# Optimization experiments

Hardware: AMD Instinct MI355X
Metric: run time of the kernel (lower is better)

Reference implementation:

```python
import jax, jax.numpy as jnp
import numpy as np

# Config (matches BlockConfig defaults for linear attention)
B, S, D = 2, 4096, 2048
H, KVH, HD, CK = 16, 8, 128, 4   # n_heads, n_kv_heads, head_dim, conv_kernel
DQK, DV = KVH * HD, H * HD       # 1024, 2048
EPS = 1e-6


def setup_inputs() -> dict:
    key = jax.random.key(0)
    ks = jax.random.split(key, 12)
    std = 0.02
    return {
        "x": jax.random.normal(ks[0], (B, S, D), jnp.float32),
        "wq": jax.random.normal(ks[1], (DQK, D), jnp.float32) * std,
        "wk": jax.random.normal(ks[2], (DQK, D), jnp.float32) * std,
        "wv": jax.random.normal(ks[3], (DV, D), jnp.float32) * std,
        "wo": jax.random.normal(ks[4], (D, DV), jnp.float32) * std,
        "q_conv_w": jax.random.normal(ks[5], (DQK, 1, CK), jnp.float32) * std,
        "k_conv_w": jax.random.normal(ks[6], (DQK, 1, CK), jnp.float32) * std,
        "alpha_w": jax.random.normal(ks[7], (H, D), jnp.float32) * std,
        "alpha_b": jnp.zeros((H,), jnp.float32),
        "beta_w": jax.random.normal(ks[8], (H, D), jnp.float32) * std,
        "beta_b": jnp.zeros((H,), jnp.float32),
        "g_w": jax.random.normal(ks[9], (DV, D), jnp.float32) * std,
        "norm_q_w": jnp.ones((HD,), jnp.float32),
        "norm_k_w": jnp.ones((HD,), jnp.float32),
    }


def _rmsnorm(x, w):
    # normalize over last dim (head_dim) in fp32, elementwise affine, no bias
    xf = x.astype(jnp.float32)
    var = jnp.mean(xf * xf, axis=-1, keepdims=True)
    return (w * xf * jax.lax.rsqrt(var + EPS)).astype(x.dtype)


def _causal_dwconv(x, w):
    # x: (B, S, C); w: (C, 1, k) depthwise; torch Conv1d padding=k-1 then [:S]
    # == left-pad (k-1, 0) cross-correlation
    y = jax.lax.conv_general_dilated(
        x.transpose(0, 2, 1), w, window_strides=(1,),
        padding=[(CK - 1, 0)], feature_group_count=w.shape[0],
        dimension_numbers=("NCH", "OIH", "NCH"))
    return y.transpose(0, 2, 1)


def reference(x, wq, wk, wv, wo, q_conv_w, k_conv_w,
              alpha_w, alpha_b, beta_w, beta_b, g_w, norm_q_w, norm_k_w):
    Q = x @ wq.T                              # (B,S,DQK)
    K = x @ wk.T                              # (B,S,DQK)
    V = x @ wv.T                              # (B,S,DV)
    Q = _causal_dwconv(Q, q_conv_w)
    K = _causal_dwconv(K, k_conv_w)
    Q = _rmsnorm(Q.reshape(B, S, KVH, HD), norm_q_w)
    K = _rmsnorm(K.reshape(B, S, KVH, HD), norm_k_w)
    V = V.reshape(B, S, H, HD)
    alpha = jax.nn.sigmoid(x @ alpha_w.T + alpha_b)              # (B,S,H)
    beta = jax.nn.sigmoid(x @ beta_w.T + beta_b) / (HD ** 0.5)   # (B,S,H)
    rep = H // KVH
    Q = jnp.repeat(Q, rep, axis=2)            # (B,S,H,HD)
    K = jnp.repeat(K, rep, axis=2)

    # time-major for scan
    Qt = Q.transpose(1, 0, 2, 3)
    Kt = K.transpose(1, 0, 2, 3)
    Vt = V.transpose(1, 0, 2, 3)
    at = alpha.transpose(1, 0, 2)
    bt = beta.transpose(1, 0, 2)

    S0 = jnp.zeros((B, H, HD, HD), x.dtype)

    def step(S_state, inp):
        q_t, k_t, v_t, a_t, b_t = inp
        pred = jnp.einsum("bhd,bhdv->bhv", k_t, S_state)
        delta = v_t - pred
        update = jnp.einsum("bhv,bhd->bhdv", delta, k_t)
        S_state = a_t[:, :, None, None] * S_state + b_t[:, :, None, None] * update
        o_t = jnp.einsum("bhd,bhdv->bhv", q_t, S_state)
        return S_state, o_t

    _, O = jax.lax.scan(step, S0, (Qt, Kt, Vt, at, bt))  # O: (S,B,H,HD)
    out = O.transpose(1, 0, 2, 3).reshape(B, S, DV)
    g = jax.nn.sigmoid(x @ g_w.T)
    return (g * out) @ wo.T
```

## Files before the change

kernel.cpp:

```cpp
#include <hip/hip_runtime.h>
#include <stdint.h>

#define DEV static __device__ __forceinline__

typedef __bf16 bf16x8 __attribute__((ext_vector_type(8)));
typedef float f32x4 __attribute__((ext_vector_type(4)));

constexpr int Bc = 2, Sc = 4096, Dc = 2048, Hc = 16, KVHc = 8, HDc = 128;
constexpr int DQKc = 1024, DVc = 2048;
constexpr int Mc = Bc * Sc;
constexpr int NCATc = 6144;
constexpr int CT = 64;
constexpr int NCH = Sc / CT;
constexpr int COEF_STRIDE = 16896;
constexpr float EPSc = 1e-6f;

DEV uint16_t f2bf(float f) {
  uint32_t u = __float_as_uint(f);
  u += 0x7FFFu + ((u >> 16) & 1u);
  return (uint16_t)(u >> 16);
}
DEV float bf2f(uint16_t h) { return __uint_as_float(((uint32_t)h) << 16); }
DEV float sigmoidf_(float z) { return 1.0f / (1.0f + __expf(-z)); }

DEV void gload16(void* lds, const void* g) {
  auto gp = (const __attribute__((address_space(1))) uint32_t*)(uintptr_t)g;
  auto lp = (__attribute__((address_space(3))) uint32_t*)(uint32_t)(uintptr_t)lds;
  __builtin_amdgcn_global_load_lds(gp, lp, 16, 0, 0);
}

__global__ __launch_bounds__(256) void cast_kernel(const float* __restrict__ src,
                                                   uint16_t* __restrict__ dst, int n4) {
  int i = blockIdx.x * blockDim.x + threadIdx.x;
  int stride = gridDim.x * blockDim.x;
  for (; i < n4; i += stride) {
    float4 v = *(const float4*)(src + (size_t)i * 4);
    ushort4 o;
    o.x = f2bf(v.x); o.y = f2bf(v.y); o.z = f2bf(v.z); o.w = f2bf(v.w);
    *(ushort4*)(dst + (size_t)i * 4) = o;
  }
}

template <typename OutT>
__global__ __launch_bounds__(512, 2) void gemm256_bt(const uint16_t* __restrict__ A,
                                                     const uint16_t* __restrict__ Bw,
                                                     OutT* __restrict__ C, int Ndim, int Kdim) {
  __shared__ uint16_t sT[2][2][2][8192];

  const int nbn = Ndim / 256;
  const int nwg = gridDim.x;
  int q = nwg >> 3, r = nwg & 7;
  int xcd = blockIdx.x & 7, lin = blockIdx.x >> 3;
  int swz = (xcd < r ? xcd * (q + 1) : r * (q + 1) + (xcd - r) * q) + lin;
  const int bm = swz / nbn, bn = swz % nbn;

  const int tid = threadIdx.x;
  const int wid = tid >> 6, lane = tid & 63;
  const int wm = wid >> 2, wn = wid & 3;
  const int lr = lane & 15;
  const int sswz8 = (((lane >> 4) ^ (lr & 3)) * 8);
  const int arow_base = wm * 128 + lr;
  const int brow_base = wn * 64 + lr;

  const uint16_t* Ab = A + (size_t)(bm * 256) * Kdim;
  const uint16_t* Bb = Bw + (size_t)(bn * 256) * Kdim;
  const int NT = Kdim >> 6;

  int srowA[2], srowB_dummy;
  (void)srowB_dummy;
  int soff[2];
  const int wbase = tid & ~63;
#pragma unroll
  for (int u = 0; u < 2; ++u) {
    int L = u * 512 + tid;
    srowA[u] = L >> 2;
    soff[u] = (((L & 3) ^ ((L >> 2) & 3)) * 8);
  }

  auto STAGE = [&](int buf, int mat, int kh, int kt) {
    const uint16_t* gb = mat == 0 ? Ab : Bb;
    uint16_t* rg = &sT[buf][mat][kh][0];
#pragma unroll
    for (int u = 0; u < 2; ++u) {
      const uint16_t* g = gb + (size_t)srowA[u] * Kdim + kt * 64 + kh * 32 + soff[u];
      gload16(rg + (u * 512 + wbase) * 8, g);
    }
  };

  f32x4 acc[8][4] = {};
  bf16x8 bfr[4];

  STAGE(0, 0, 0, 0); STAGE(0, 1, 0, 0);
  STAGE(0, 0, 1, 0); STAGE(0, 1, 1, 0);
  STAGE(1, 0, 0, 1); STAGE(1, 1, 0, 1);
  asm volatile("s_waitcnt vmcnt(4)" ::: "memory");
  __builtin_amdgcn_s_barrier();

  for (int kt = 0; kt < NT; ++kt) {
    const int buf = kt & 1;
    const uint16_t* aR0 = &sT[buf][0][0][0];
    const uint16_t* bR0 = &sT[buf][1][0][0];
    const uint16_t* aR1 = &sT[buf][0][1][0];
    const uint16_t* bR1 = &sT[buf][1][1][0];

    {
      bf16x8 af[4];
#pragma unroll
      for (int m = 0; m < 4; ++m)
        af[m] = *(const bf16x8*)&aR0[(arow_base + m * 16) * 32 + sswz8];
#pragma unroll
      for (int n = 0; n < 4; ++n)
        bfr[n] = *(const bf16x8*)&bR0[(brow_base + n * 16) * 32 + sswz8];
      if (kt + 1 < NT) STAGE(buf ^ 1, 0, 1, kt + 1);
      __builtin_amdgcn_s_setprio(1);
#pragma unroll
      for (int m = 0; m < 4; ++m)
#pragma unroll
        for (int n = 0; n < 4; ++n)
          acc[m][n] = __builtin_amdgcn_mfma_f32_16x16x32_bf16(af[m], bfr[n], acc[m][n], 0, 0, 0);
      __builtin_amdgcn_s_setprio(0);
      __builtin_amdgcn_s_barrier();
    }
    {
      bf16x8 af[4];
#pragma unroll
      for (int m = 0; m < 4; ++m)
        af[m] = *(const bf16x8*)&aR0[(arow_base + (m + 4) * 16) * 32 + sswz8];
      if (kt + 1 < NT) STAGE(buf ^ 1, 1, 1, kt + 1);
      __builtin_amdgcn_s_setprio(1);
#pragma unroll
      for (int m = 0; m < 4; ++m)
#pragma unroll
        for (int n = 0; n < 4; ++n)
          acc[m + 4][n] = __builtin_amdgcn_mfma_f32_16x16x32_bf16(af[m], bfr[n], acc[m + 4][n], 0, 0, 0);
      __builtin_amdgcn_s_setprio(0);
      __builtin_amdgcn_s_barrier();
    }
    {
      bf16x8 af[4];
#pragma unroll
      for (int m = 0; m < 4; ++m)
        af[m] = *(const bf16x8*)&aR1[(arow_base + m * 16) * 32 + sswz8];
#pragma unroll
      for (int n = 0; n < 4; ++n)
        bfr[n] = *(const bf16x8*)&bR1[(brow_base + n * 16) * 32 + sswz8];
      if (kt + 2 < NT) STAGE(buf, 0, 0, kt + 2);
      __builtin_amdgcn_s_setprio(1);
#pragma unroll
      for (int m = 0; m < 4; ++m)
#pragma unroll
        for (int n = 0; n < 4; ++n)
          acc[m][n] = __builtin_amdgcn_mfma_f32_16x16x32_bf16(af[m], bfr[n], acc[m][n], 0, 0, 0);
      __builtin_amdgcn_s_setprio(0);
      __builtin_amdgcn_s_barrier();
    }
    {
      bf16x8 af[4];
#pragma unroll
      for (int m = 0; m < 4; ++m)
        af[m] = *(const bf16x8*)&aR1[(arow_base + (m + 4) * 16) * 32 + sswz8];
      if (kt + 2 < NT) STAGE(buf, 1, 0, kt + 2);
      __builtin_amdgcn_s_setprio(1);
#pragma unroll
      for (int m = 0; m < 4; ++m)
#pragma unroll
        for (int n = 0; n < 4; ++n)
          acc[m + 4][n] = __builtin_amdgcn_mfma_f32_16x16x32_bf16(af[m], bfr[n], acc[m + 4][n], 0, 0, 0);
      __builtin_amdgcn_s_setprio(0);
    }
    if (kt + 1 < NT) {
      if (kt + 2 < NT)
        asm volatile("s_waitcnt vmcnt(4)" ::: "memory");
      else
        asm volatile("s_waitcnt vmcnt(0)" ::: "memory");
      __builtin_amdgcn_s_barrier();
    }
  }

  const int r0 = (lane >> 4) * 4;
#pragma unroll
  for (int m = 0; m < 8; ++m)
#pragma unroll
    for (int n = 0; n < 4; ++n) {
      int col = bn * 256 + wn * 64 + n * 16 + lr;
#pragma unroll
      for (int j = 0; j < 4; ++j) {
        int row = bm * 256 + wm * 128 + m * 16 + r0 + j;
        float val = acc[m][n][j];
        if constexpr (sizeof(OutT) == 2)
          C[(size_t)row * Ndim + col] = (OutT)f2bf(val);
        else
          C[(size_t)row * Ndim + col] = (OutT)val;
      }
    }
}

__global__ __launch_bounds__(256) void alphabeta_kernel(const float* __restrict__ x,
                                                        const float* __restrict__ aw,
                                                        const float* __restrict__ abias,
                                                        const float* __restrict__ bw,
                                                        const float* __restrict__ bbias,
                                                        float* __restrict__ out) {
  __shared__ float xrow[Dc];
  const int row = blockIdx.x;
  const float* xp = x + (size_t)row * Dc;
  for (int i = threadIdx.x; i < Dc; i += 256) xrow[i] = xp[i];
  __syncthreads();
  const int o = threadIdx.x >> 3, lg = threadIdx.x & 7;
  const float* wrow = (o < 16) ? (aw + (size_t)o * Dc) : (bw + (size_t)(o - 16) * Dc);
  float s = 0.f;
  for (int i = lg * 4; i < Dc; i += 32) {
    float4 xv = *(const float4*)&xrow[i];
    float4 wv = *(const float4*)&wrow[i];
    s += xv.x * wv.x + xv.y * wv.y + xv.z * wv.z + xv.w * wv.w;
  }
  s += __shfl_xor(s, 1); s += __shfl_xor(s, 2); s += __shfl_xor(s, 4);
  if (lg == 0) {
    float bias = (o < 16) ? abias[o] : bbias[o - 16];
    float sig = sigmoidf_(s + bias);
    if (o >= 16) sig *= 0.08838834764831845f;
    out[(size_t)row * 32 + o] = sig;
  }
}

__global__ __launch_bounds__(256) void convnorm_kernel(const uint16_t* __restrict__ C1,
                                                       const float* __restrict__ qcw,
                                                       const float* __restrict__ kcw,
                                                       const float* __restrict__ nqw,
                                                       const float* __restrict__ nkw,
                                                       uint16_t* __restrict__ Qn,
                                                       uint16_t* __restrict__ Kn) {
  const int wid = blockIdx.x * 4 + (threadIdx.x >> 6);
  const int lane = threadIdx.x & 63;
  const int kvh = wid & 7;
  const int t = (wid >> 3) & (Sc - 1);
  const int b = wid >> 15;
  float qv[2], kv[2];
#pragma unroll
  for (int half = 0; half < 2; ++half) {
    const int c = lane + half * 64;
    const int ch = kvh * HDc + c;
    float qs = 0.f, ks = 0.f;
#pragma unroll
    for (int j = 0; j < 4; ++j) {
      int tt = t - 3 + j;
      if (tt >= 0) {
        size_t rb = (size_t)(b * Sc + tt) * NCATc;
        qs = fmaf(bf2f(C1[rb + ch]), qcw[ch * 4 + j], qs);
        ks = fmaf(bf2f(C1[rb + 1024 + ch]), kcw[ch * 4 + j], ks);
      }
    }
    qv[half] = qs; kv[half] = ks;
  }
  float sq = qv[0] * qv[0] + qv[1] * qv[1];
  float sk = kv[0] * kv[0] + kv[1] * kv[1];
#pragma unroll
  for (int m = 1; m < 64; m <<= 1) { sq += __shfl_xor(sq, m); sk += __shfl_xor(sk, m); }
  const float rq = rsqrtf(sq * (1.f / HDc) + EPSc);
  const float rk = rsqrtf(sk * (1.f / HDc) + EPSc);
#pragma unroll
  for (int half = 0; half < 2; ++half) {
    const int c = lane + half * 64;
    size_t oidx = (size_t)(b * Sc + t) * DQKc + kvh * HDc + c;
    Qn[oidx] = f2bf(nqw[c] * qv[half] * rq);
    Kn[oidx] = f2bf(nkw[c] * kv[half] * rk);
  }
}

__global__ __launch_bounds__(256) void scores_kernel(const uint16_t* __restrict__ Qn,
                                                     const uint16_t* __restrict__ Kn,
                                                     const float* __restrict__ ab,
                                                     uint8_t* __restrict__ coef) {
  __shared__ __align__(16) char smem[72192];
  uint16_t* sK = (uint16_t*)smem;
  float* Wtf = (float*)smem;
  uint16_t* sQ = (uint16_t*)(smem + 17408);
  uint16_t* sM2 = sQ;
  uint16_t* Msh = (uint16_t*)(smem + 34816);
  uint16_t* Msl = (uint16_t*)(smem + 44032);
  uint16_t* Thh = (uint16_t*)(smem + 53248);
  uint16_t* Thl = (uint16_t*)(smem + 62464);
  float* Lb = (float*)(smem + 71680);
  float* bbv = Lb + 64;

  const int bid = blockIdx.x;
  const int c = bid & 63, h = (bid >> 6) & 15, b = bid >> 10;
  const int kh = h >> 1;
  const int t0 = c * 64;
  const int tid = threadIdx.x;
  const int w = tid >> 6, l = tid & 63, lr = l & 15, lk = (l >> 4) * 8;
  const int sr = tid >> 2, sq2 = tid & 3;

  uint8_t* cbase = coef + (size_t)((b * Hc + h) * NCH + c) * COEF_STRIDE;
  uint16_t* m2out = (uint16_t*)cbase;
  uint16_t* eout = (uint16_t*)(cbase + 8192);
  float* gout = (float*)(cbase + 16384);

  {
    const size_t rb = (size_t)(b * Sc + t0 + sr) * DQKc + kh * HDc + sq2 * 32;
#pragma unroll
    for (int u = 0; u < 4; ++u) {
      uint4 kv = *(const uint4*)(Kn + rb + u * 8);
      uint4 qv = *(const uint4*)(Qn + rb + u * 8);
      *(uint4*)&sK[sr * 136 + sq2 * 32 + u * 8] = kv;
      *(uint4*)&sQ[sr * 136 + sq2 * 32 + u * 8] = qv;
    }
  }
  if (tid < 64) {
    const float* abp = ab + (size_t)(b * Sc + t0 + tid) * 32 + h;
    float av = fmaxf(abp[0], 1e-30f);
    float bv = abp[16];
    float la = log2f(av);
    float L = la;
#pragma unroll
    for (int off = 1; off < 64; off <<= 1) {
      float up = __shfl_up(L, off, 64);
      if (tid >= off) L += up;
    }
    Lb[tid] = L; bbv[tid] = bv;
    gout[tid] = exp2f(L - la);
    gout[64 + tid] = exp2f(L);
  }
  __syncthreads();

  f32x4 kkacc[4] = {}, qkacc[4] = {};
#pragma unroll
  for (int k0 = 0; k0 < 128; k0 += 32) {
    bf16x8 ka = *(const bf16x8*)&sK[(16 * w + lr) * 136 + k0 + lk];
    bf16x8 qa = *(const bf16x8*)&sQ[(16 * w + lr) * 136 + k0 + lk];
#pragma unroll
    for (int n = 0; n < 4; ++n) {
      bf16x8 kb = *(const bf16x8*)&sK[(16 * n + lr) * 136 + k0 + lk];
      kkacc[n] = __builtin_amdgcn_mfma_f32_16x16x32_bf16(ka, kb, kkacc[n], 0, 0, 0);
      qkacc[n] = __builtin_amdgcn_mfma_f32_16x16x32_bf16(qa, kb, qkacc[n], 0, 0, 0);
    }
  }
  __syncthreads();

  const float L63 = Lb[63];
#pragma unroll
  for (int n = 0; n < 4; ++n)
#pragma unroll
    for (int jj = 0; jj < 4; ++jj) {
      const int i = 16 * w + (l >> 4) * 4 + jj;
      const int j = 16 * n + lr;
      float Li = Lb[i];
      float Lim = (i > 0) ? Lb[(i > 0) ? i - 1 : 0] : 0.f;
      float Lj = Lb[j];
      float bj = bbv[j];
      float wv = (j < i) ? exp2f(Lim - Lj) * bj * kkacc[n][jj] : 0.f;
      Wtf[j * 68 + i] = wv;
      float ms = (j <= i) ? exp2f(Li - Lj) * bj * qkacc[n][jj] : 0.f;
      uint16_t mh = f2bf(ms);
      Msh[i * 72 + j] = mh;
      Msl[i * 72 + j] = f2bf(ms - bf2f(mh));
    }
  __syncthreads();

  if (tid < 64) {
    float acc[64];
#pragma unroll
    for (int i = 0; i < 64; ++i) acc[i] = 0.f;
#pragma unroll
    for (int ll = 0; ll < 64; ++ll) {
      float xl = ((tid == ll) ? 1.f : 0.f) - acc[ll];
      uint16_t xh = f2bf(xl);
      Thh[tid * 72 + ll] = xh;
      Thl[tid * 72 + ll] = f2bf(xl - bf2f(xh));
#pragma unroll
      for (int i = ll + 1; i < 64; ++i)
        acc[i] = fmaf(Wtf[ll * 68 + i], xl, acc[i]);
    }
  }
  __syncthreads();

  f32x4 m2acc[4] = {};
#pragma unroll
  for (int k0 = 0; k0 < 64; k0 += 32) {
    bf16x8 ah = *(const bf16x8*)&Msh[(16 * w + lr) * 72 + k0 + lk];
    bf16x8 al = *(const bf16x8*)&Msl[(16 * w + lr) * 72 + k0 + lk];
#pragma unroll
    for (int n = 0; n < 4; ++n) {
      bf16x8 bh = *(const bf16x8*)&Thh[(16 * n + lr) * 72 + k0 + lk];
      bf16x8 bl = *(const bf16x8*)&Thl[(16 * n + lr) * 72 + k0 + lk];
      m2acc[n] = __builtin_amdgcn_mfma_f32_16x16x32_bf16(ah, bh, m2acc[n], 0, 0, 0);
      m2acc[n] = __builtin_amdgcn_mfma_f32_16x16x32_bf16(ah, bl, m2acc[n], 0, 0, 0);
      m2acc[n] = __builtin_amdgcn_mfma_f32_16x16x32_bf16(al, bh, m2acc[n], 0, 0, 0);
    }
  }
#pragma unroll
  for (int n = 0; n < 4; ++n)
#pragma unroll
    for (int jj = 0; jj < 4; ++jj) {
      const int i = 16 * w + (l >> 4) * 4 + jj;
      const int j = 16 * n + lr;
      sM2[i * 72 + j] = f2bf(m2acc[n][jj]);
    }
  {
    const int i2 = tid >> 2, tq = tid & 3;
    float gC = exp2f(L63 - Lb[i2]) * bbv[i2];
    uint32_t pk[8];
#pragma unroll
    for (int p = 0; p < 8; ++p) {
      int t1 = tq * 16 + p * 2;
      float e0 = gC * (bf2f(Thh[(t1 + 0) * 72 + i2]) + bf2f(Thl[(t1 + 0) * 72 + i2]));
      float e1 = gC * (bf2f(Thh[(t1 + 1) * 72 + i2]) + bf2f(Thl[(t1 + 1) * 72 + i2]));
      pk[p] = (uint32_t)f2bf(e0) | ((uint32_t)f2bf(e1) << 16);
    }
    uint4 o0 = make_uint4(pk[0], pk[1], pk[2], pk[3]);
    uint4 o1 = make_uint4(pk[4], pk[5], pk[6], pk[7]);
    *(uint4*)(eout + i2 * 64 + tq * 16) = o0;
    *(uint4*)(eout + i2 * 64 + tq * 16 + 8) = o1;
  }
  __syncthreads();
  {
    const int i2 = tid >> 2, tq = tid & 3;
    uint4 a0 = *(const uint4*)&sM2[i2 * 72 + tq * 16];
    uint4 a1 = *(const uint4*)&sM2[i2 * 72 + tq * 16 + 8];
    *(uint4*)(m2out + i2 * 64 + tq * 16) = a0;
    *(uint4*)(m2out + i2 * 64 + tq * 16 + 8) = a1;
  }
}

__global__ __launch_bounds__(256) void scan_kernel(const uint16_t* __restrict__ Qn,
                                                   const uint16_t* __restrict__ Kn,
                                                   const uint16_t* __restrict__ C1,
                                                   const uint8_t* __restrict__ coef,
                                                   float* __restrict__ O) {
  __shared__ __align__(16) uint16_t Kb[64 * 136];
  __shared__ __align__(16) uint16_t Qb[64 * 136];
  __shared__ __align__(16) uint16_t Ktb[128 * 72];
  __shared__ __align__(16) uint16_t M2b[64 * 72];
  __shared__ __align__(16) uint16_t Eb[64 * 72];
  __shared__ __align__(16) uint16_t Vb[64 * 24];
  __shared__ __align__(16) uint16_t Rt[16 * 72];
  __shared__ __align__(16) uint16_t D2t[16 * 72];
  __shared__ __align__(16) uint16_t Sh[16 * 136];
  __shared__ __align__(16) uint16_t Slo[16 * 136];
  __shared__ float gABb[128];

  const int bid = blockIdx.x;
  const int kh = bid & 7;
  const int j2 = bid >> 3;
  const int sl = j2 >> 2;
  const int b = (j2 >> 1) & 1;
  const int h = kh * 2 + (j2 & 1);
  const int ch0 = (b * Hc + h) * NCH;

  const int tid = threadIdx.x;
  const int w = tid >> 6, l = tid & 63;
  const int lr = l & 15, lk = (l >> 4) * 8;
  const int row0 = 16 * w + (l >> 4) * 4;
  const int vcol = lr;
  const int sr = tid >> 2, sq2 = tid & 3;

  const size_t kqbase = (size_t)(b * Sc) * DQKc + kh * HDc;
  const size_t vbase = (size_t)(b * Sc) * NCATc + 2048 + h * HDc + sl * 16;
  float* Ob = O + (size_t)(b * Sc) * DVc + h * HDc + sl * 16 + vcol;

  float sreg[2][4] = {};
  uint4 kA[4], kB[4], qA[4], qB[4];

  auto LOADS = [&](int cn, uint4 (&kd)[4], uint4 (&qd)[4], uint4 (&m2d)[2], uint4 (&ed)[2],
                   uint4& vd, float& gd) {
    const size_t rb = kqbase + (size_t)(cn * CT + sr) * DQKc + sq2 * 32;
#pragma unroll
    for (int u = 0; u < 4; ++u) {
      kd[u] = *(const uint4*)(Kn + rb + u * 8);
      qd[u] = *(const uint4*)(Qn + rb + u * 8);
    }
    const uint16_t* cf = (const uint16_t*)(coef + (size_t)(ch0 + cn) * COEF_STRIDE);
#pragma unroll
    for (int e = 0; e < 2; ++e) {
      m2d[e] = *(const uint4*)(cf + sr * 64 + sq2 * 16 + e * 8);
      ed[e] = *(const uint4*)(cf + 4096 + sr * 64 + sq2 * 16 + e * 8);
    }
    if (tid < 128) {
      vd = *(const uint4*)(C1 + vbase + (size_t)(cn * CT + (tid >> 1)) * NCATc + (tid & 1) * 8);
      gd = ((const float*)(cf + 8192))[tid];
    }
  };
  auto WSTAGE = [&](const uint4 (&kd)[4], const uint4 (&qd)[4], const uint4 (&m2d)[2],
                    const uint4 (&ed)[2], const uint4& vd, const float& gd) {
#pragma unroll
    for (int u = 0; u < 4; ++u) {
      *(uint4*)&Kb[sr * 136 + sq2 * 32 + u * 8] = kd[u];
      *(uint4*)&Qb[sr * 136 + sq2 * 32 + u * 8] = qd[u];
    }
#pragma unroll
    for (int e = 0; e < 2; ++e) {
      *(uint4*)&M2b[sr * 72 + sq2 * 16 + e * 8] = m2d[e];
      *(uint4*)&Eb[sr * 72 + sq2 * 16 + e * 8] = ed[e];
    }
    if (tid < 128) {
      *(uint4*)&Vb[(tid >> 1) * 24 + (tid & 1) * 8] = vd;
      gABb[tid] = gd;
    }
  };

  auto CHUNK = [&](int c, bool pre, uint4 (&kcur)[4], uint4 (&knxt)[4],
                   uint4 (&qcur)[4], uint4 (&qnxt)[4]) {
    uint4 m2d[2], ed[2]; uint4 vd; float gd = 0.f;
    if (pre) LOADS(c + 1, knxt, qnxt, m2d, ed, vd, gd);

#pragma unroll
    for (int u = 0; u < 4; ++u) {
      const int c0 = sq2 * 32 + u * 8;
      uint32_t x0 = kcur[u].x, x1 = kcur[u].y, x2 = kcur[u].z, x3 = kcur[u].w;
      Ktb[(c0 + 0) * 72 + sr] = (uint16_t)x0; Ktb[(c0 + 1) * 72 + sr] = (uint16_t)(x0 >> 16);
      Ktb[(c0 + 2) * 72 + sr] = (uint16_t)x1; Ktb[(c0 + 3) * 72 + sr] = (uint16_t)(x1 >> 16);
      Ktb[(c0 + 4) * 72 + sr] = (uint16_t)x2; Ktb[(c0 + 5) * 72 + sr] = (uint16_t)(x2 >> 16);
      Ktb[(c0 + 6) * 72 + sr] = (uint16_t)x3; Ktb[(c0 + 7) * 72 + sr] = (uint16_t)(x3 >> 16);
    }
    f32x4 accP = {0, 0, 0, 0}, accPq = {0, 0, 0, 0};
#pragma unroll
    for (int k0 = 0; k0 < 128; k0 += 32) {
      bf16x8 ka = *(const bf16x8*)&Kb[(16 * w + lr) * 136 + k0 + lk];
      bf16x8 qa = *(const bf16x8*)&Qb[(16 * w + lr) * 136 + k0 + lk];
      bf16x8 shf = *(const bf16x8*)&Sh[lr * 136 + k0 + lk];
      bf16x8 slf = *(const bf16x8*)&Slo[lr * 136 + k0 + lk];
      accP = __builtin_amdgcn_mfma_f32_16x16x32_bf16(ka, shf, accP, 0, 0, 0);
      accP = __builtin_amdgcn_mfma_f32_16x16x32_bf16(ka, slf, accP, 0, 0, 0);
      accPq = __builtin_amdgcn_mfma_f32_16x16x32_bf16(qa, shf, accPq, 0, 0, 0);
      accPq = __builtin_amdgcn_mfma_f32_16x16x32_bf16(qa, slf, accPq, 0, 0, 0);
    }
    {
      float rv[4];
#pragma unroll
      for (int j = 0; j < 4; ++j) {
        float vv = bf2f(Vb[(row0 + j) * 24 + vcol]);
        float ga = gABb[row0 + j];
        rv[j] = vv - ga * accP[j];
      }
      uint32_t r01 = (uint32_t)f2bf(rv[0]) | ((uint32_t)f2bf(rv[1]) << 16);
      uint32_t r23 = (uint32_t)f2bf(rv[2]) | ((uint32_t)f2bf(rv[3]) << 16);
      *(uint2*)&Rt[vcol * 72 + row0] = make_uint2(r01, r23);
    }
    __syncthreads();

    f32x4 accD2 = {0, 0, 0, 0}, accO = {0, 0, 0, 0};
#pragma unroll
    for (int k0 = 0; k0 < 64; k0 += 32) {
      bf16x8 rb8 = *(const bf16x8*)&Rt[lr * 72 + k0 + lk];
      bf16x8 ea = *(const bf16x8*)&Eb[(16 * w + lr) * 72 + k0 + lk];
      bf16x8 ma = *(const bf16x8*)&M2b[(16 * w + lr) * 72 + k0 + lk];
      accD2 = __builtin_amdgcn_mfma_f32_16x16x32_bf16(ea, rb8, accD2, 0, 0, 0);
      accO = __builtin_amdgcn_mfma_f32_16x16x32_bf16(ma, rb8, accO, 0, 0, 0);
    }
    {
      float* op = Ob + (size_t)(c * CT) * DVc;
#pragma unroll
      for (int j = 0; j < 4; ++j) {
        float o = gABb[64 + row0 + j] * accPq[j] + accO[j];
        op[(size_t)(row0 + j) * DVc] = o;
      }
      uint32_t d01 = (uint32_t)f2bf(accD2[0]) | ((uint32_t)f2bf(accD2[1]) << 16);
      uint32_t d23 = (uint32_t)f2bf(accD2[2]) | ((uint32_t)f2bf(accD2[3]) << 16);
      *(uint2*)&D2t[vcol * 72 + row0] = make_uint2(d01, d23);
    }
    __syncthreads();

    const float gT = gABb[127];
    f32x4 accY[2] = {{0, 0, 0, 0}, {0, 0, 0, 0}};
#pragma unroll
    for (int k0 = 0; k0 < 64; k0 += 32) {
      bf16x8 db = *(const bf16x8*)&D2t[lr * 72 + k0 + lk];
      bf16x8 ka0 = *(const bf16x8*)&Ktb[(32 * w + lr) * 72 + k0 + lk];
      bf16x8 ka1 = *(const bf16x8*)&Ktb[(32 * w + 16 + lr) * 72 + k0 + lk];
      accY[0] = __builtin_amdgcn_mfma_f32_16x16x32_bf16(ka0, db, accY[0], 0, 0, 0);
      accY[1] = __builtin_amdgcn_mfma_f32_16x16x32_bf16(ka1, db, accY[1], 0, 0, 0);
    }
#pragma unroll
    for (int m = 0; m < 2; ++m) {
      uint16_t hi[4], lo[4];
#pragma unroll
      for (int j = 0; j < 4; ++j) {
        float s = gT * sreg[m][j] + accY[m][j];
        sreg[m][j] = s;
        hi[j] = f2bf(s);
        lo[j] = f2bf(s - bf2f(hi[j]));
      }
      const int dk0 = 32 * w + m * 16 + (l >> 4) * 4;
      *(uint2*)&Sh[vcol * 136 + dk0] =
          make_uint2((uint32_t)hi[0] | ((uint32_t)hi[1] << 16),
                     (uint32_t)hi[2] | ((uint32_t)hi[3] << 16));
      *(uint2*)&Slo[vcol * 136 + dk0] =
          make_uint2((uint32_t)lo[0] | ((uint32_t)lo[1] << 16),
                     (uint32_t)lo[2] | ((uint32_t)lo[3] << 16));
    }
    if (pre) WSTAGE(knxt, qnxt, m2d, ed, vd, gd);
    __syncthreads();
  };

  {
    uint4 m2d[2], ed[2]; uint4 vd; float gd = 0.f;
    LOADS(0, kA, qA, m2d, ed, vd, gd);
    WSTAGE(kA, qA, m2d, ed, vd, gd);
  }
  for (int i = tid; i < 16 * 136; i += 256) { Sh[i] = 0; Slo[i] = 0; }
  __syncthreads();

  for (int c2 = 0; c2 < NCH; c2 += 2) {
    CHUNK(c2, true, kA, kB, qA, qB);
    CHUNK(c2 + 1, c2 + 2 < NCH, kB, kA, qB, qA);
  }
}

__global__ __launch_bounds__(256) void gmul_kernel(const uint16_t* __restrict__ C1,
                                                   const float* __restrict__ O,
                                                   uint16_t* __restrict__ gOb) {
  int i = blockIdx.x * blockDim.x + threadIdx.x;
  const int n4 = Mc * DVc / 4;
  const int stride = gridDim.x * blockDim.x;
  for (; i < n4; i += stride) {
    int idx = i * 4;
    int row = idx >> 11;
    int col = idx & (DVc - 1);
    ushort4 gr = *(const ushort4*)&C1[(size_t)row * NCATc + 4096 + col];
    float4 ov = *(const float4*)&O[idx];
    ushort4 r;
    r.x = f2bf(sigmoidf_(bf2f(gr.x)) * ov.x);
    r.y = f2bf(sigmoidf_(bf2f(gr.y)) * ov.y);
    r.z = f2bf(sigmoidf_(bf2f(gr.z)) * ov.z);
    r.w = f2bf(sigmoidf_(bf2f(gr.w)) * ov.w);
    *(ushort4*)&gOb[idx] = r;
  }
}

extern "C" void kernel_launch(void* const* d_in, const int* in_sizes, int n_in,
                              void* d_out, int out_size, void* d_ws, size_t ws_size,
                              hipStream_t stream) {
  (void)in_sizes; (void)n_in; (void)out_size; (void)ws_size;
  const float* x     = (const float*)d_in[0];
  const float* wq    = (const float*)d_in[1];
  const float* wk    = (const float*)d_in[2];
  const float* wv    = (const float*)d_in[3];
  const float* wo    = (const float*)d_in[4];
  const float* qcw   = (const float*)d_in[5];
  const float* kcw   = (const float*)d_in[6];
  const float* aw    = (const float*)d_in[7];
  const float* abias = (const float*)d_in[8];
  const float* bw    = (const float*)d_in[9];
  const float* bbias = (const float*)d_in[10];
  const float* gw    = (const float*)d_in[11];
  const float* nqw   = (const float*)d_in[12];
  const float* nkw   = (const float*)d_in[13];

  uint8_t* ws = (uint8_t*)d_ws;
  uint16_t* xb   = (uint16_t*)(ws);
  uint16_t* wcat = (uint16_t*)(ws + 33554432);
  uint16_t* wob  = (uint16_t*)(ws + 58720256);
  uint16_t* c1   = (uint16_t*)(ws + 67108864);
  float*    abuf = (float*)   (ws + 167772160);
  uint16_t* qn   = (uint16_t*)(ws + 168820736);
  uint16_t* kn   = (uint16_t*)(ws + 185597952);
  uint8_t*  cofs = (uint8_t*)ws;
  uint16_t* gob  = xb;
  float* obuf = (float*)d_out;

  cast_kernel<<<2048, 256, 0, stream>>>(x, xb, Mc * Dc / 4);
  cast_kernel<<<1024, 256, 0, stream>>>(wq, wcat, DQKc * Dc / 4);
  cast_kernel<<<1024, 256, 0, stream>>>(wk, wcat + DQKc * Dc, DQKc * Dc / 4);
  cast_kernel<<<1024, 256, 0, stream>>>(wv, wcat + 2 * DQKc * Dc, DVc * Dc / 4);
  cast_kernel<<<1024, 256, 0, stream>>>(gw, wcat + 2 * DQKc * Dc + DVc * Dc, DVc * Dc / 4);
  cast_kernel<<<1024, 256, 0, stream>>>(wo, wob, DVc * Dc / 4);

  gemm256_bt<uint16_t><<<768, 512, 0, stream>>>(xb, wcat, c1, NCATc, Dc);
  alphabeta_kernel<<<8192, 256, 0, stream>>>(x, aw, abias, bw, bbias, abuf);
  convnorm_kernel<<<16384, 256, 0, stream>>>(c1, qcw, kcw, nqw, nkw, qn, kn);
  scores_kernel<<<2048, 256, 0, stream>>>(qn, kn, abuf, cofs);
  scan_kernel<<<256, 256, 0, stream>>>(qn, kn, c1, cofs, obuf);
  gmul_kernel<<<2048, 256, 0, stream>>>(c1, obuf, gob);
  gemm256_bt<float><<<256, 512, 0, stream>>>(gob, wob, (float*)d_out, DVc, Dc);
}
```

Measured before the change: 791.6 us.

## Fuse gating into scan, share K across head pairs, double-buffer K transpose

The sigmoid gate multiply moves into the scan kernel's output path, which writes bf16 gated output in place over the g columns of C1. The final GEMM reads those columns directly through a new lda stride, so gmul_kernel and the fp32 O round trip go away. scores_kernel now handles both query heads that share one KV head per block, loading Q/K once and using more LDS. alphabeta processes 8 rows per block. The scan double-buffers the K transpose scatter and overlaps it with MFMA work, and the GEMM LDS swizzle pattern is changed. These changes add LDS pressure and strided 2-byte gate loads inside the scan.

```diff
diff --git a/kernel.cpp b/kernel.cpp
--- a/kernel.cpp
+++ b/kernel.cpp
@@ -44,7 +44,8 @@
 template <typename OutT>
 __global__ __launch_bounds__(512, 2) void gemm256_bt(const uint16_t* __restrict__ A,
                                                      const uint16_t* __restrict__ Bw,
-                                                     OutT* __restrict__ C, int Ndim, int Kdim) {
+                                                     OutT* __restrict__ C, int Ndim, int Kdim,
+                                                     int lda) {
   __shared__ uint16_t sT[2][2][2][8192];
 
   const int nbn = Ndim / 256;
@@ -58,31 +59,31 @@
   const int wid = tid >> 6, lane = tid & 63;
   const int wm = wid >> 2, wn = wid & 3;
   const int lr = lane & 15;
-  const int sswz8 = (((lane >> 4) ^ (lr & 3)) * 8);
+  const int sswz8 = (((lane >> 4) ^ ((lr >> 1) & 3)) * 8);
   const int arow_base = wm * 128 + lr;
   const int brow_base = wn * 64 + lr;
 
-  const uint16_t* Ab = A + (size_t)(bm * 256) * Kdim;
+  const uint16_t* Ab = A + (size_t)(bm * 256) * lda;
   const uint16_t* Bb = Bw + (size_t)(bn * 256) * Kdim;
   const int NT = Kdim >> 6;
 
-  int srowA[2], srowB_dummy;
-  (void)srowB_dummy;
+  int srowA[2];
   int soff[2];
   const int wbase = tid & ~63;
 #pragma unroll
   for (int u = 0; u < 2; ++u) {
     int L = u * 512 + tid;
     srowA[u] = L >> 2;
-    soff[u] = (((L & 3) ^ ((L >> 2) & 3)) * 8);
+    soff[u] = (((L & 3) ^ ((L >> 3) & 3)) * 8);
   }
 
   auto STAGE = [&](int buf, int mat, int kh, int kt) {
     const uint16_t* gb = mat == 0 ? Ab : Bb;
+    const int ld = mat == 0 ? lda : Kdim;
     uint16_t* rg = &sT[buf][mat][kh][0];
 #pragma unroll
     for (int u = 0; u < 2; ++u) {
-      const uint16_t* g = gb + (size_t)srowA[u] * Kdim + kt * 64 + kh * 32 + soff[u];
+      const uint16_t* g = gb + (size_t)srowA[u] * ld + kt * 64 + kh * 32 + soff[u];
       gload16(rg + (u * 512 + wbase) * 8, g);
     }
   };
@@ -201,26 +202,26 @@
                                                         const float* __restrict__ bw,
                                                         const float* __restrict__ bbias,
                                                         float* __restrict__ out) {
-  __shared__ float xrow[Dc];
-  const int row = blockIdx.x;
-  const float* xp = x + (size_t)row * Dc;
-  for (int i = threadIdx.x; i < Dc; i += 256) xrow[i] = xp[i];
+  __shared__ float xs[8 * Dc];
+  const int row0 = blockIdx.x * 8;
+  const float* xp = x + (size_t)row0 * Dc;
+  for (int i = threadIdx.x; i < 8 * Dc / 4; i += 256)
+    *(float4*)&xs[i * 4] = *(const float4*)(xp + (size_t)i * 4);
   __syncthreads();
-  const int o = threadIdx.x >> 3, lg = threadIdx.x & 7;
+  const int r = threadIdx.x >> 5, o = threadIdx.x & 31;
   const float* wrow = (o < 16) ? (aw + (size_t)o * Dc) : (bw + (size_t)(o - 16) * Dc);
+  const float* xr = &xs[r * Dc];
   float s = 0.f;
-  for (int i = lg * 4; i < Dc; i += 32) {
-    float4 xv = *(const float4*)&xrow[i];
-    float4 wv = *(const float4*)&wrow[i];
+#pragma unroll 4
+  for (int k = 0; k < Dc; k += 4) {
+    float4 wv = *(const float4*)(wrow + k);
+    float4 xv = *(const float4*)(xr + k);
     s += xv.x * wv.x + xv.y * wv.y + xv.z * wv.z + xv.w * wv.w;
   }
-  s += __shfl_xor(s, 1); s += __shfl_xor(s, 2); s += __shfl_xor(s, 4);
-  if (lg == 0) {
-    float bias = (o < 16) ? abias[o] : bbias[o - 16];
-    float sig = sigmoidf_(s + bias);
-    if (o >= 16) sig *= 0.08838834764831845f;
-    out[(size_t)row * 32 + o] = sig;
-  }
+  float bias = (o < 16) ? abias[o] : bbias[o - 16];
+  float sig = sigmoidf_(s + bias);
+  if (o >= 16) sig *= 0.08838834764831845f;
+  out[(size_t)(row0 + r) * 32 + o] = sig;
 }
 
 __global__ __launch_bounds__(256) void convnorm_kernel(const uint16_t* __restrict__ C1,
@@ -271,30 +272,29 @@
                                                      const uint16_t* __restrict__ Kn,
                                                      const float* __restrict__ ab,
                                                      uint8_t* __restrict__ coef) {
-  __shared__ __align__(16) char smem[72192];
+  __shared__ __align__(16) char smem[109568];
   uint16_t* sK = (uint16_t*)smem;
-  float* Wtf = (float*)smem;
   uint16_t* sQ = (uint16_t*)(smem + 17408);
-  uint16_t* sM2 = sQ;
-  uint16_t* Msh = (uint16_t*)(smem + 34816);
-  uint16_t* Msl = (uint16_t*)(smem + 44032);
-  uint16_t* Thh = (uint16_t*)(smem + 53248);
-  uint16_t* Thl = (uint16_t*)(smem + 62464);
-  float* Lb = (float*)(smem + 71680);
-  float* bbv = Lb + 64;
+  uint16_t* sM2 = (uint16_t*)smem;
+  float* Lb = (float*)(smem + 108544);
+  float* bbv = Lb + 128;
+
+  auto Wt_p  = [&](int hd) { return (float*)(smem + hd * 17408); };
+  auto Msh_p = [&](int hd) { return (uint16_t*)(smem + 34816 + hd * 18432); };
+  auto Msl_p = [&](int hd) { return (uint16_t*)(smem + 44032 + hd * 18432); };
+  auto Thh_p = [&](int hd) { return (uint16_t*)(smem + 71680 + hd * 18432); };
+  auto Thl_p = [&](int hd) { return (uint16_t*)(smem + 80896 + hd * 18432); };
 
   const int bid = blockIdx.x;
-  const int c = bid & 63, h = (bid >> 6) & 15, b = bid >> 10;
-  const int kh = h >> 1;
+  const int c = bid & 63, kh = (bid >> 6) & 7, b = bid >> 9;
   const int t0 = c * 64;
   const int tid = threadIdx.x;
   const int w = tid >> 6, l = tid & 63, lr = l & 15, lk = (l >> 4) * 8;
   const int sr = tid >> 2, sq2 = tid & 3;
 
-  uint8_t* cbase = coef + (size_t)((b * Hc + h) * NCH + c) * COEF_STRIDE;
-  uint16_t* m2out = (uint16_t*)cbase;
-  uint16_t* eout = (uint16_t*)(cbase + 8192);
-  float* gout = (float*)(cbase + 16384);
+  auto cb_p = [&](int hd) {
+    return coef + (size_t)((b * Hc + kh * 2 + hd) * NCH + c) * COEF_STRIDE;
+  };
 
   {
     const size_t rb = (size_t)(b * Sc + t0 + sr) * DQKc + kh * HDc + sq2 * 32;
@@ -306,8 +306,9 @@
       *(uint4*)&sQ[sr * 136 + sq2 * 32 + u * 8] = qv;
     }
   }
-  if (tid < 64) {
-    const float* abp = ab + (size_t)(b * Sc + t0 + tid) * 32 + h;
+  if (tid < 128) {
+    const int hd = tid >> 6, tt = tid & 63;
+    const float* abp = ab + (size_t)(b * Sc + t0 + tt) * 32 + (kh * 2 + hd);
     float av = fmaxf(abp[0], 1e-30f);
     float bv = abp[16];
     float la = log2f(av);
@@ -315,11 +316,12 @@
 #pragma unroll
     for (int off = 1; off < 64; off <<= 1) {
       float up = __shfl_up(L, off, 64);
-      if (tid >= off) L += up;
-    }
-    Lb[tid] = L; bbv[tid] = bv;
-    gout[tid] = exp2f(L - la);
-    gout[64 + tid] = exp2f(L);
+      if (tt >= off) L += up;
+    }
+    Lb[hd * 64 + tt] = L; bbv[hd * 64 + tt] = bv;
+    float* gout = (float*)(cb_p(hd) + 16384);
+    gout[tt] = exp2f(L - la);
+    gout[64 + tt] = exp2f(L);
   }
   __syncthreads();
 
@@ -337,99 +339,121 @@
   }
   __syncthreads();
 
-  const float L63 = Lb[63];
-#pragma unroll
-  for (int n = 0; n < 4; ++n)
-#pragma unroll
-    for (int jj = 0; jj < 4; ++jj) {
-      const int i = 16 * w + (l >> 4) * 4 + jj;
-      const int j = 16 * n + lr;
-      float Li = Lb[i];
-      float Lim = (i > 0) ? Lb[(i > 0) ? i - 1 : 0] : 0.f;
-      float Lj = Lb[j];
-      float bj = bbv[j];
-      float wv = (j < i) ? exp2f(Lim - Lj) * bj * kkacc[n][jj] : 0.f;
-      Wtf[j * 68 + i] = wv;
-      float ms = (j <= i) ? exp2f(Li - Lj) * bj * qkacc[n][jj] : 0.f;
-      uint16_t mh = f2bf(ms);
-      Msh[i * 72 + j] = mh;
-      Msl[i * 72 + j] = f2bf(ms - bf2f(mh));
-    }
+#pragma unroll
+  for (int hd = 0; hd < 2; ++hd) {
+    float* Wt = Wt_p(hd);
+    uint16_t* Mh = Msh_p(hd);
+    uint16_t* Ml = Msl_p(hd);
+    const float* Lh = Lb + hd * 64;
+    const float* bh = bbv + hd * 64;
+#pragma unroll
+    for (int n = 0; n < 4; ++n)
+#pragma unroll
+      for (int jj = 0; jj < 4; ++jj) {
+        const int i = 16 * w + (l >> 4) * 4 + jj;
+        const int j = 16 * n + lr;
+        float Li = Lh[i];
+        float Lim = (i > 0) ? Lh[(i > 0) ? i - 1 : 0] : 0.f;
+        float Lj = Lh[j];
+        float bj = bh[j];
+        float wv = (j < i) ? exp2f(Lim - Lj) * bj * kkacc[n][jj] : 0.f;
+        Wt[j * 68 + i] = wv;
+        float ms = (j <= i) ? exp2f(Li - Lj) * bj * qkacc[n][jj] : 0.f;
+        uint16_t mh = f2bf(ms);
+        Mh[i * 72 + j] = mh;
+        Ml[i * 72 + j] = f2bf(ms - bf2f(mh));
+      }
+  }
   __syncthreads();
 
-  if (tid < 64) {
+  if (tid < 128) {
+    const int hd = tid >> 6, col = tid & 63;
+    float* Wt = Wt_p(hd);
+    uint16_t* Th = Thh_p(hd);
+    uint16_t* Tl = Thl_p(hd);
     float acc[64];
 #pragma unroll
     for (int i = 0; i < 64; ++i) acc[i] = 0.f;
 #pragma unroll
     for (int ll = 0; ll < 64; ++ll) {
-      float xl = ((tid == ll) ? 1.f : 0.f) - acc[ll];
+      float xl = ((col == ll) ? 1.f : 0.f) - acc[ll];
       uint16_t xh = f2bf(xl);
-      Thh[tid * 72 + ll] = xh;
-      Thl[tid * 72 + ll] = f2bf(xl - bf2f(xh));
+      Th[col * 72 + ll] = xh;
+      Tl[col * 72 + ll] = f2bf(xl - bf2f(xh));
 #pragma unroll
       for (int i = ll + 1; i < 64; ++i)
-        acc[i] = fmaf(Wtf[ll * 68 + i], xl, acc[i]);
+        acc[i] = fmaf(Wt[ll * 68 + i], xl, acc[i]);
     }
   }
   __syncthreads();
 
-  f32x4 m2acc[4] = {};
-#pragma unroll
-  for (int k0 = 0; k0 < 64; k0 += 32) {
-    bf16x8 ah = *(const bf16x8*)&Msh[(16 * w + lr) * 72 + k0 + lk];
-    bf16x8 al = *(const bf16x8*)&Msl[(16 * w + lr) * 72 + k0 + lk];
-#pragma unroll
-    for (int n = 0; n < 4; ++n) {
-      bf16x8 bh = *(const bf16x8*)&Thh[(16 * n + lr) * 72 + k0 + lk];
-      bf16x8 bl = *(const bf16x8*)&Thl[(16 * n + lr) * 72 + k0 + lk];
-      m2acc[n] = __builtin_amdgcn_mfma_f32_16x16x32_bf16(ah, bh, m2acc[n], 0, 0, 0);
-      m2acc[n] = __builtin_amdgcn_mfma_f32_16x16x32_bf16(ah, bl, m2acc[n], 0, 0, 0);
-      m2acc[n] = __builtin_amdgcn_mfma_f32_16x16x32_bf16(al, bh, m2acc[n], 0, 0, 0);
-    }
-  }
-#pragma unroll
-  for (int n = 0; n < 4; ++n)
-#pragma unroll
-    for (int jj = 0; jj < 4; ++jj) {
-      const int i = 16 * w + (l >> 4) * 4 + jj;
-      const int j = 16 * n + lr;
-      sM2[i * 72 + j] = f2bf(m2acc[n][jj]);
-    }
-  {
-    const int i2 = tid >> 2, tq = tid & 3;
-    float gC = exp2f(L63 - Lb[i2]) * bbv[i2];
-    uint32_t pk[8];
-#pragma unroll
-    for (int p = 0; p < 8; ++p) {
-      int t1 = tq * 16 + p * 2;
-      float e0 = gC * (bf2f(Thh[(t1 + 0) * 72 + i2]) + bf2f(Thl[(t1 + 0) * 72 + i2]));
-      float e1 = gC * (bf2f(Thh[(t1 + 1) * 72 + i2]) + bf2f(Thl[(t1 + 1) * 72 + i2]));
-      pk[p] = (uint32_t)f2bf(e0) | ((uint32_t)f2bf(e1) << 16);
-    }
-    uint4 o0 = make_uint4(pk[0], pk[1], pk[2], pk[3]);
-    uint4 o1 = make_uint4(pk[4], pk[5], pk[6], pk[7]);
-    *(uint4*)(eout + i2 * 64 + tq * 16) = o0;
-    *(uint4*)(eout + i2 * 64 + tq * 16 + 8) = o1;
-  }
-  __syncthreads();
-  {
-    const int i2 = tid >> 2, tq = tid & 3;
-    uint4 a0 = *(const uint4*)&sM2[i2 * 72 + tq * 16];
-    uint4 a1 = *(const uint4*)&sM2[i2 * 72 + tq * 16 + 8];
-    *(uint4*)(m2out + i2 * 64 + tq * 16) = a0;
-    *(uint4*)(m2out + i2 * 64 + tq * 16 + 8) = a1;
+  for (int hd = 0; hd < 2; ++hd) {
+    uint16_t* Mh = Msh_p(hd);
+    uint16_t* Ml = Msl_p(hd);
+    uint16_t* Th = Thh_p(hd);
+    uint16_t* Tl = Thl_p(hd);
+    uint16_t* m2out = (uint16_t*)cb_p(hd);
+    uint16_t* eout = (uint16_t*)(cb_p(hd) + 8192);
+    const float* Lh = Lb + hd * 64;
+    const float* bh = bbv + hd * 64;
+    const float L63 = Lh[63];
+
+    {
+      const int i2 = tid >> 2, tq = tid & 3;
+      float gC = exp2f(L63 - Lh[i2]) * bh[i2];
+      uint32_t pk[8];
+#pragma unroll
+      for (int p = 0; p < 8; ++p) {
+        int t1 = tq * 16 + p * 2;
+        float e0 = gC * (bf2f(Th[(t1 + 0) * 72 + i2]) + bf2f(Tl[(t1 + 0) * 72 + i2]));
+        float e1 = gC * (bf2f(Th[(t1 + 1) * 72 + i2]) + bf2f(Tl[(t1 + 1) * 72 + i2]));
+        pk[p] = (uint32_t)f2bf(e0) | ((uint32_t)f2bf(e1) << 16);
+      }
+      *(uint4*)(eout + i2 * 64 + tq * 16) = make_uint4(pk[0], pk[1], pk[2], pk[3]);
+      *(uint4*)(eout + i2 * 64 + tq * 16 + 8) = make_uint4(pk[4], pk[5], pk[6], pk[7]);
+    }
+
+    f32x4 m2acc[4] = {};
+#pragma unroll
+    for (int k0 = 0; k0 < 64; k0 += 32) {
+      bf16x8 ah = *(const bf16x8*)&Mh[(16 * w + lr) * 72 + k0 + lk];
+      bf16x8 al = *(const bf16x8*)&Ml[(16 * w + lr) * 72 + k0 + lk];
+#pragma unroll
+      for (int n = 0; n < 4; ++n) {
+        bf16x8 bhf = *(const bf16x8*)&Th[(16 * n + lr) * 72 + k0 + lk];
+        bf16x8 blf = *(const bf16x8*)&Tl[(16 * n + lr) * 72 + k0 + lk];
+        m2acc[n] = __builtin_amdgcn_mfma_f32_16x16x32_bf16(ah, bhf, m2acc[n], 0, 0, 0);
+        m2acc[n] = __builtin_amdgcn_mfma_f32_16x16x32_bf16(ah, blf, m2acc[n], 0, 0, 0);
+        m2acc[n] = __builtin_amdgcn_mfma_f32_16x16x32_bf16(al, bhf, m2acc[n], 0, 0, 0);
+      }
+    }
+#pragma unroll
+    for (int n = 0; n < 4; ++n)
+#pragma unroll
+      for (int jj = 0; jj < 4; ++jj) {
+        const int i = 16 * w + (l >> 4) * 4 + jj;
+        const int j = 16 * n + lr;
+        sM2[i * 72 + j] = f2bf(m2acc[n][jj]);
+      }
+    __syncthreads();
+    {
+      const int i2 = tid >> 2, tq = tid & 3;
+      uint4 a0 = *(const uint4*)&sM2[i2 * 72 + tq * 16];
+      uint4 a1 = *(const uint4*)&sM2[i2 * 72 + tq * 16 + 8];
+      *(uint4*)(m2out + i2 * 64 + tq * 16) = a0;
+      *(uint4*)(m2out + i2 * 64 + tq * 16 + 8) = a1;
+    }
+    __syncthreads();
   }
 }
 
 __global__ __launch_bounds__(256) void scan_kernel(const uint16_t* __restrict__ Qn,
                                                    const uint16_t* __restrict__ Kn,
-                                                   const uint16_t* __restrict__ C1,
-                                                   const uint8_t* __restrict__ coef,
-                                                   float* __restrict__ O) {
+                                                   uint16_t* C1,
+                                                   const uint8_t* __restrict__ coef) {
   __shared__ __align__(16) uint16_t Kb[64 * 136];
   __shared__ __align__(16) uint16_t Qb[64 * 136];
-  __shared__ __align__(16) uint16_t Ktb[128 * 72];
+  __shared__ __align__(16) uint16_t Ktb[2][128 * 72];
   __shared__ __align__(16) uint16_t M2b[64 * 72];
   __shared__ __align__(16) uint16_t Eb[64 * 72];
   __shared__ __align__(16) uint16_t Vb[64 * 24];
@@ -456,13 +480,14 @@
 
   const size_t kqbase = (size_t)(b * Sc) * DQKc + kh * HDc;
   const size_t vbase = (size_t)(b * Sc) * NCATc + 2048 + h * HDc + sl * 16;
-  float* Ob = O + (size_t)(b * Sc) * DVc + h * HDc + sl * 16 + vcol;
+  uint16_t* Gb = C1 + (size_t)(b * Sc) * NCATc + 4096 + h * HDc + sl * 16 + vcol;
 
   float sreg[2][4] = {};
   uint4 kA[4], kB[4], qA[4], qB[4];
+  ushort4 gv0, gv1;
 
   auto LOADS = [&](int cn, uint4 (&kd)[4], uint4 (&qd)[4], uint4 (&m2d)[2], uint4 (&ed)[2],
-                   uint4& vd, float& gd) {
+                   uint4& vd, float& gd, ushort4& gvd) {
     const size_t rb = kqbase + (size_t)(cn * CT + sr) * DQKc + sq2 * 32;
 #pragma unroll
     for (int u = 0; u < 4; ++u) {
@@ -479,6 +504,11 @@
       vd = *(const uint4*)(C1 + vbase + (size_t)(cn * CT + (tid >> 1)) * NCATc + (tid & 1) * 8);
       gd = ((const float*)(cf + 8192))[tid];
     }
+    const uint16_t* gpre = Gb + (size_t)(cn * CT) * NCATc;
+    gvd.x = gpre[(size_t)(row0 + 0) * NCATc];
+    gvd.y = gpre[(size_t)(row0 + 1) * NCATc];
+    gvd.z = gpre[(size_t)(row0 + 2) * NCATc];
+    gvd.w = gpre[(size_t)(row0 + 3) * NCATc];
   };
   auto WSTAGE = [&](const uint4 (&kd)[4], const uint4 (&qd)[4], const uint4 (&m2d)[2],
                     const uint4 (&ed)[2], const uint4& vd, const float& gd) {
@@ -497,21 +527,22 @@
       gABb[tid] = gd;
     }
   };
+  auto SCAT = [&](uint16_t* Kt, const uint4 (&kd)[4], int u) {
+    const int c0 = sq2 * 32 + u * 8;
+    uint32_t x0 = kd[u].x, x1 = kd[u].y, x2 = kd[u].z, x3 = kd[u].w;
+    Kt[(c0 + 0) * 72 + sr] = (uint16_t)x0; Kt[(c0 + 1) * 72 + sr] = (uint16_t)(x0 >> 16);
+    Kt[(c0 + 2) * 72 + sr] = (uint16_t)x1; Kt[(c0 + 3) * 72 + sr] = (uint16_t)(x1 >> 16);
+    Kt[(c0 + 4) * 72 + sr] = (uint16_t)x2; Kt[(c0 + 5) * 72 + sr] = (uint16_t)(x2 >> 16);
+    Kt[(c0 + 6) * 72 + sr] = (uint16_t)x3; Kt[(c0 + 7) * 72 + sr] = (uint16_t)(x3 >> 16);
+  };
 
   auto CHUNK = [&](int c, bool pre, uint4 (&kcur)[4], uint4 (&knxt)[4],
-                   uint4 (&qcur)[4], uint4 (&qnxt)[4]) {
+                   uint4 (&qcur)[4], uint4 (&qnxt)[4], ushort4& gvcur, ushort4& gvnxt) {
     uint4 m2d[2], ed[2]; uint4 vd; float gd = 0.f;
-    if (pre) LOADS(c + 1, knxt, qnxt, m2d, ed, vd, gd);
-
-#pragma unroll
-    for (int u = 0; u < 4; ++u) {
-      const int c0 = sq2 * 32 + u * 8;
-      uint32_t x0 = kcur[u].x, x1 = kcur[u].y, x2 = kcur[u].z, x3 = kcur[u].w;
-      Ktb[(c0 + 0) * 72 + sr] = (uint16_t)x0; Ktb[(c0 + 1) * 72 + sr] = (uint16_t)(x0 >> 16);
-      Ktb[(c0 + 2) * 72 + sr] = (uint16_t)x1; Ktb[(c0 + 3) * 72 + sr] = (uint16_t)(x1 >> 16);
-      Ktb[(c0 + 4) * 72 + sr] = (uint16_t)x2; Ktb[(c0 + 5) * 72 + sr] = (uint16_t)(x2 >> 16);
-      Ktb[(c0 + 6) * 72 + sr] = (uint16_t)x3; Ktb[(c0 + 7) * 72 + sr] = (uint16_t)(x3 >> 16);
-    }
+    if (pre) LOADS(c + 1, knxt, qnxt, m2d, ed, vd, gd, gvnxt);
+    const uint16_t* Ktc = Ktb[c & 1];
+    uint16_t* Ktn = Ktb[(c + 1) & 1];
+
     f32x4 accP = {0, 0, 0, 0}, accPq = {0, 0, 0, 0};
 #pragma unroll
     for (int k0 = 0; k0 < 128; k0 += 32) {
@@ -547,12 +578,15 @@
       accD2 = __builtin_amdgcn_mfma_f32_16x16x32_bf16(ea, rb8, accD2, 0, 0, 0);
       accO = __builtin_amdgcn_mfma_f32_16x16x32_bf16(ma, rb8, accO, 0, 0, 0);
     }
-    {
-      float* op = Ob + (size_t)(c * CT) * DVc;
+    if (pre) { SCAT(Ktn, knxt, 0); SCAT(Ktn, knxt, 1); }
+    {
+      uint16_t* gp = Gb + (size_t)(c * CT) * NCATc;
+      uint16_t gvv[4] = {gvcur.x, gvcur.y, gvcur.z, gvcur.w};
 #pragma unroll
       for (int j = 0; j < 4; ++j) {
         float o = gABb[64 + row0 + j] * accPq[j] + accO[j];
-        op[(size_t)(row0 + j) * DVc] = o;
+        float gg = sigmoidf_(bf2f(gvv[j]));
+        gp[(size_t)(row0 + j) * NCATc] = f2bf(o * gg);
       }
       uint32_t d01 = (uint32_t)f2bf(accD2[0]) | ((uint32_t)f2bf(accD2[1]) << 16);
       uint32_t d23 = (uint32_t)f2bf(accD2[2]) | ((uint32_t)f2bf(accD2[3]) << 16);
@@ -565,11 +599,12 @@
 #pragma unroll
     for (int k0 = 0; k0 < 64; k0 += 32) {
       bf16x8 db = *(const bf16x8*)&D2t[lr * 72 + k0 + lk];
-      bf16x8 ka0 = *(const bf16x8*)&Ktb[(32 * w + lr) * 72 + k0 + lk];
-      bf16x8 ka1 = *(const bf16x8*)&Ktb[(32 * w + 16 + lr) * 72 + k0 + lk];
+      bf16x8 ka0 = *(const bf16x8*)&Ktc[(32 * w + lr) * 72 + k0 + lk];
+      bf16x8 ka1 = *(const bf16x8*)&Ktc[(32 * w + 16 + lr) * 72 + k0 + lk];
       accY[0] = __builtin_amdgcn_mfma_f32_16x16x32_bf16(ka0, db, accY[0], 0, 0, 0);
       accY[1] = __builtin_amdgcn_mfma_f32_16x16x32_bf16(ka1, db, accY[1], 0, 0, 0);
     }
+    if (pre) { SCAT(Ktn, knxt, 2); SCAT(Ktn, knxt, 3); }
 #pragma unroll
     for (int m = 0; m < 2; ++m) {
       uint16_t hi[4], lo[4];
@@ -594,36 +629,17 @@
 
   {
     uint4 m2d[2], ed[2]; uint4 vd; float gd = 0.f;
-    LOADS(0, kA, qA, m2d, ed, vd, gd);
+    LOADS(0, kA, qA, m2d, ed, vd, gd, gv0);
     WSTAGE(kA, qA, m2d, ed, vd, gd);
+#pragma unroll
+    for (int u = 0; u < 4; ++u) SCAT(Ktb[0], kA, u);
   }
   for (int i = tid; i < 16 * 136; i += 256) { Sh[i] = 0; Slo[i] = 0; }
   __syncthreads();
 
   for (int c2 = 0; c2 < NCH; c2 += 2) {
-    CHUNK(c2, true, kA, kB, qA, qB);
-    CHUNK(c2 + 1, c2 + 2 < NCH, kB, kA, qB, qA);
-  }
-}
-
-__global__ __launch_bounds__(256) void gmul_kernel(const uint16_t* __restrict__ C1,
-                                                   const float* __restrict__ O,
-                                                   uint16_t* __restrict__ gOb) {
-  int i = blockIdx.x * blockDim.x + threadIdx.x;
-  const int n4 = Mc * DVc / 4;
-  const int stride = gridDim.x * blockDim.x;
-  for (; i < n4; i += stride) {
-    int idx = i * 4;
-    int row = idx >> 11;
-    int col = idx & (DVc - 1);
-    ushort4 gr = *(const ushort4*)&C1[(size_t)row * NCATc + 4096 + col];
-    float4 ov = *(const float4*)&O[idx];
-    ushort4 r;
-    r.x = f2bf(sigmoidf_(bf2f(gr.x)) * ov.x);
-    r.y = f2bf(sigmoidf_(bf2f(gr.y)) * ov.y);
-    r.z = f2bf(sigmoidf_(bf2f(gr.z)) * ov.z);
-    r.w = f2bf(sigmoidf_(bf2f(gr.w)) * ov.w);
-    *(ushort4*)&gOb[idx] = r;
+    CHUNK(c2, true, kA, kB, qA, qB, gv0, gv1);
+    CHUNK(c2 + 1, c2 + 2 < NCH, kB, kA, qB, qA, gv1, gv0);
   }
 }
 
@@ -655,8 +671,6 @@
   uint16_t* qn   = (uint16_t*)(ws + 168820736);
   uint16_t* kn   = (uint16_t*)(ws + 185597952);
   uint8_t*  cofs = (uint8_t*)ws;
-  uint16_t* gob  = xb;
-  float* obuf = (float*)d_out;
 
   cast_kernel<<<2048, 256, 0, stream>>>(x, xb, Mc * Dc / 4);
   cast_kernel<<<1024, 256, 0, stream>>>(wq, wcat, DQKc * Dc / 4);
@@ -665,11 +679,10 @@
   cast_kernel<<<1024, 256, 0, stream>>>(gw, wcat + 2 * DQKc * Dc + DVc * Dc, DVc * Dc / 4);
   cast_kernel<<<1024, 256, 0, stream>>>(wo, wob, DVc * Dc / 4);
 
-  gemm256_bt<uint16_t><<<768, 512, 0, stream>>>(xb, wcat, c1, NCATc, Dc);
-  alphabeta_kernel<<<8192, 256, 0, stream>>>(x, aw, abias, bw, bbias, abuf);
+  gemm256_bt<uint16_t><<<768, 512, 0, stream>>>(xb, wcat, c1, NCATc, Dc, Dc);
+  alphabeta_kernel<<<1024, 256, 0, stream>>>(x, aw, abias, bw, bbias, abuf);
   convnorm_kernel<<<16384, 256, 0, stream>>>(c1, qcw, kcw, nqw, nkw, qn, kn);
-  scores_kernel<<<2048, 256, 0, stream>>>(qn, kn, abuf, cofs);
-  scan_kernel<<<256, 256, 0, stream>>>(qn, kn, c1, cofs, obuf);
-  gmul_kernel<<<2048, 256, 0, stream>>>(c1, obuf, gob);
-  gemm256_bt<float><<<256, 512, 0, stream>>>(gob, wob, (float*)d_out, DVc, Dc);
-}
+  scores_kernel<<<1024, 256, 0, stream>>>(qn, kn, abuf, cofs);
+  scan_kernel<<<256, 256, 0, stream>>>(qn, kn, c1, cofs);
+  gemm256_bt<float><<<256, 512, 0, stream>>>(c1 + 4096, wob, (float*)d_out, DVc, Dc, NCATc);
+}
```

After: 881.5 us. +11.4%, slower.
